# Kernel tuning notes

Measured on AMD Instinct MI355X. Metric: run time of the kernel, lower is better.

Reference implementation:

```python
import jax, jax.numpy as jnp
import numpy as np

EPS = 1e-5

def _ln(x):
    # LayerNorm over last dim, no affine (elementwise_affine=False)
    mu = jnp.mean(x, axis=-1, keepdims=True)
    var = jnp.mean(jnp.square(x - mu), axis=-1, keepdims=True)
    return (x - mu) * jax.lax.rsqrt(var + EPS)

def setup_inputs() -> dict:
    key = jax.random.key(0)
    ks = jax.random.split(key, 6)
    B, L, D = 2, 2048, 2048
    s = 1.0 / np.sqrt(D)
    return {
        "x": jax.random.normal(ks[0], (B, L, D), jnp.float32),
        "Wq": jax.random.normal(ks[1], (D, D), jnp.float32) * s,
        "Wk": jax.random.normal(ks[2], (D, D), jnp.float32) * s,
        "Wv": jax.random.normal(ks[3], (D, D), jnp.float32) * s,
        "Wo": jax.random.normal(ks[4], (D, D), jnp.float32) * s,
        "bo": jnp.zeros((D,), jnp.float32),
    }

def reference(x, Wq, Wk, Wv, Wo, bo):
    B, L, D = x.shape
    H = 16
    hd = D // H
    q = (x @ Wq.T).reshape(B, L, H, hd)
    k = (x @ Wk.T).reshape(B, L, H, hd)
    v = (x @ Wv.T).reshape(B, L, H, hd)
    q = _ln(q)
    k = _ln(k)
    scores = jnp.einsum('blhd,bshd->bhls', q, k) / np.sqrt(hd)
    causal = jnp.tril(jnp.ones((L, L), bool))  # [L, L]
    scores = jnp.where(causal[None, None], scores, -jnp.inf)
    probs = jax.nn.softmax(scores, axis=-1)
    out = jnp.einsum('bhls,bshd->blhd', probs, v).reshape(B, L, D)
    return out @ Wo.T + bo
```

## Files before the change

kernel.cpp:

```cpp
#include <hip/hip_runtime.h>
#include <stdint.h>

typedef unsigned short u16;
typedef __attribute__((ext_vector_type(8))) unsigned short u16x8;
typedef __attribute__((ext_vector_type(8))) __bf16 bf16x8;
typedef __attribute__((ext_vector_type(4))) float f32x4;
typedef __attribute__((ext_vector_type(8))) float f32x8;

#define AS_G __attribute__((address_space(1)))
#define AS_L __attribute__((address_space(3)))

static __device__ __forceinline__ void gload_lds16(const u16* g, u16* l) {
  __builtin_amdgcn_global_load_lds((AS_G void*)(u16*)g, (AS_L void*)l, 16, 0, 0);
}

static __device__ __forceinline__ u16 f2bf(float f) {
  union { float f; unsigned u; } v; v.f = f;
  return (u16)((v.u + 0x7FFFu + ((v.u >> 16) & 1u)) >> 16);
}
static __device__ __forceinline__ float bf2f(u16 b) {
  union { unsigned u; float f; } v; v.u = ((unsigned)b) << 16;
  return v.f;
}
static __device__ __forceinline__ u16 f2bf_trunc(float f) {
  union { float f; unsigned u; } v; v.f = f;
  return (u16)(v.u >> 16);
}

#define BAR() do { asm volatile("" ::: "memory"); __builtin_amdgcn_s_barrier(); asm volatile("" ::: "memory"); } while (0)

__global__ __launch_bounds__(256) void cast_all(
    const float* __restrict__ x, const float* __restrict__ Wq,
    const float* __restrict__ Wk, const float* __restrict__ Wv,
    const float* __restrict__ Wo,
    u16* __restrict__ xb, u16* __restrict__ Wcat, u16* __restrict__ Wob)
{
  const int NX = (4096 * 2048) / 8;
  const int NW = (2048 * 2048) / 8;
  const int total = NX + 4 * NW;
  for (int i = blockIdx.x * 256 + threadIdx.x; i < total; i += gridDim.x * 256) {
    const float* src; u16* dst; int idx;
    if (i < NX)               { src = x;  dst = xb;                 idx = i; }
    else if (i < NX + NW)     { src = Wq; dst = Wcat;               idx = i - NX; }
    else if (i < NX + 2*NW)   { src = Wk; dst = Wcat + 2048*2048;   idx = i - NX - NW; }
    else if (i < NX + 3*NW)   { src = Wv; dst = Wcat + 2*2048*2048; idx = i - NX - 2*NW; }
    else                      { src = Wo; dst = Wob;                idx = i - NX - 3*NW; }
    f32x8 v = *(const f32x8*)(src + (size_t)idx * 8);
    u16x8 o;
    #pragma unroll
    for (int e = 0; e < 8; e++) o[e] = f2bf(v[e]);
    *(u16x8*)(dst + (size_t)idx * 8) = o;
  }
}

__global__ __launch_bounds__(512, 1) void gemm_qkv(
    const u16* __restrict__ A, const u16* __restrict__ B,
    u16* __restrict__ QK, u16* __restrict__ Vt, int K)
{
  __shared__ char SM[98304];
  u16* Asb = (u16*)SM;
  u16* Bsb = (u16*)(SM + 32768);
  const int tid = threadIdx.x, lane = tid & 63, wid = tid >> 6;
  const int wm = wid >> 2, wn = wid & 3;
  const int row0 = blockIdx.x * 128, col0 = blockIdx.y * 256;
  const int NT = K >> 6;

  const int sr  = tid >> 3;
  const int scb = ((tid & 7) * 16) ^ ((sr & 7) << 4);

  auto stA = [&](int buf, int t, int u) {
    const u16* src = A + (size_t)(row0 + u * 64 + sr) * K + t * 64 + (scb >> 1);
    gload_lds16(src, Asb + buf * 8192 + u * 4096 + wid * 512);
  };
  auto stB = [&](int buf, int t, int u) {
    const u16* src = B + (size_t)(col0 + u * 64 + sr) * K + t * 64 + (scb >> 1);
    gload_lds16(src, Bsb + buf * 16384 + u * 4096 + wid * 512);
  };
  auto ldA = [&](int buf, int mf, int k) {
    int ra = wm * 64 + mf * 16 + (lane & 15);
    int bc = (k * 64 + ((lane >> 4) << 4)) ^ ((ra & 7) << 4);
    return *(const bf16x8*)((const char*)Asb + buf * 16384 + ra * 128 + bc);
  };
  auto ldB = [&](int buf, int nf, int k) {
    int rb = wn * 64 + nf * 16 + (lane & 15);
    int bc = (k * 64 + ((lane >> 4) << 4)) ^ ((rb & 7) << 4);
    return *(const bf16x8*)((const char*)Bsb + buf * 32768 + rb * 128 + bc);
  };

  f32x4 acc[4][4] = {};
  bf16x8 breg[4][2];

#define MFMA_PH(mf, x0, x1) \
  do { __builtin_amdgcn_s_setprio(1); \
    _Pragma("unroll") \
    for (int nf = 0; nf < 4; ++nf) { \
      acc[mf][nf] = __builtin_amdgcn_mfma_f32_16x16x32_bf16(x0, breg[nf][0], acc[mf][nf], 0, 0, 0); \
      acc[mf][nf] = __builtin_amdgcn_mfma_f32_16x16x32_bf16(x1, breg[nf][1], acc[mf][nf], 0, 0, 0); \
    } \
    __builtin_amdgcn_s_setprio(0); } while (0)

  stA(0, 0, 0); stA(0, 0, 1);
  stB(0, 0, 0); stB(0, 0, 1); stB(0, 0, 2); stB(0, 0, 3);
  stB(1, 1, 0); stB(1, 1, 1); stB(1, 1, 2); stB(1, 1, 3);
  asm volatile("s_waitcnt vmcnt(4)" ::: "memory");
  BAR();

  for (int it = 0; it < NT / 2; ++it) {
    const int t1  = 2 * it + 1;
    const int pf0 = (2 * it + 2 < NT) ? (2 * it + 2) : (NT - 1);
    const int pf1 = (2 * it + 3 < NT) ? (2 * it + 3) : (NT - 1);
    #pragma unroll
    for (int hf = 0; hf < 2; ++hf) {
      const int cb = hf;
      #pragma unroll
      for (int nf = 0; nf < 4; ++nf) { breg[nf][0] = ldB(cb, nf, 0); breg[nf][1] = ldB(cb, nf, 1); }
      bf16x8 a0 = ldA(cb, 0, 0), a1 = ldA(cb, 0, 1);
      BAR();
      if (hf == 0) { stA(1, t1, 0); stA(1, t1, 1); } else { stA(0, pf0, 0); stA(0, pf0, 1); }
      MFMA_PH(0, a0, a1);
      a0 = ldA(cb, 1, 0); a1 = ldA(cb, 1, 1);
      BAR();
      if (hf == 0) { stB(0, pf0, 0); stB(0, pf0, 1); } else { stB(1, pf1, 0); stB(1, pf1, 1); }
      MFMA_PH(1, a0, a1);
      a0 = ldA(cb, 2, 0); a1 = ldA(cb, 2, 1);
      BAR();
      if (hf == 0) { stB(0, pf0, 2); stB(0, pf0, 3); } else { stB(1, pf1, 2); stB(1, pf1, 3); }
      MFMA_PH(2, a0, a1);
      a0 = ldA(cb, 3, 0); a1 = ldA(cb, 3, 1);
      MFMA_PH(3, a0, a1);
      asm volatile("s_waitcnt vmcnt(4)" ::: "memory");
      BAR();
    }
  }
  asm volatile("s_waitcnt vmcnt(0)" ::: "memory");
  BAR();

  if (col0 < 4096) {
    float* red = (float*)SM;
    #pragma unroll
    for (int mf = 0; mf < 4; ++mf) {
      #pragma unroll
      for (int e = 0; e < 4; ++e) {
        float s = acc[mf][0][e] + acc[mf][1][e] + acc[mf][2][e] + acc[mf][3][e];
        float q = acc[mf][0][e]*acc[mf][0][e] + acc[mf][1][e]*acc[mf][1][e]
                + acc[mf][2][e]*acc[mf][2][e] + acc[mf][3][e]*acc[mf][3][e];
        #pragma unroll
        for (int m = 1; m < 16; m <<= 1) { s += __shfl_xor(s, m); q += __shfl_xor(q, m); }
        if ((lane & 15) == 0) {
          int rl = mf * 16 + (lane >> 4) * 4 + e;
          red[wid * 128 + rl * 2]     = s;
          red[wid * 128 + rl * 2 + 1] = q;
        }
      }
    }
    BAR();
    const float mul = (col0 < 2048) ? (0.08838834764831845f * 1.4426950408889634f) : 1.0f;
    #pragma unroll
    for (int mf = 0; mf < 4; ++mf) {
      #pragma unroll
      for (int e = 0; e < 4; ++e) {
        int rl = mf * 16 + (lane >> 4) * 4 + e;
        float s = red[wid * 128 + rl * 2]     + red[(wid ^ 1) * 128 + rl * 2];
        float q = red[wid * 128 + rl * 2 + 1] + red[(wid ^ 1) * 128 + rl * 2 + 1];
        float mu = s * (1.f / 128.f);
        float var = q * (1.f / 128.f) - mu * mu;
        float rstd = rsqrtf(var + 1e-5f) * mul;
        int r = row0 + wm * 64 + rl;
        #pragma unroll
        for (int nf = 0; nf < 4; ++nf) {
          int c = col0 + wn * 64 + nf * 16 + (lane & 15);
          QK[(size_t)r * 4096 + c] = f2bf((acc[mf][nf][e] - mu) * rstd);
        }
      }
    }
  } else {
    u16* T = (u16*)SM;
    #pragma unroll
    for (int mf = 0; mf < 4; ++mf) {
      #pragma unroll
      for (int nf = 0; nf < 4; ++nf) {
        #pragma unroll
        for (int e = 0; e < 4; ++e) {
          int r = wm * 64 + mf * 16 + (lane >> 4) * 4 + e;
          int c = wn * 64 + nf * 16 + (lane & 15);
          T[c * 136 + r] = f2bf(acc[mf][nf][e]);
        }
      }
    }
    BAR();
    const int dr = tid >> 1, half = tid & 1;
    const int dg = col0 - 4096 + dr;
    const int h = dg >> 7, dd = dg & 127;
    const int b = row0 >> 11;
    const int lb = (row0 & 2047) + half * 64;
    u16* dst = Vt + ((size_t)((b * 16 + h) * 128 + dd)) * 2048 + lb;
    const u16* srcT = T + dr * 136 + half * 64;
    #pragma unroll
    for (int j = 0; j < 8; ++j)
      *(u16x8*)(dst + j * 8) = *(const u16x8*)(srcT + j * 8);
  }
#undef MFMA_PH
}

__global__ __launch_bounds__(512, 2) void gemm_ao(
    const u16* __restrict__ A, const u16* __restrict__ B,
    float* __restrict__ C, const float* __restrict__ bias,
    int M, int N, int K)
{
  __shared__ u16 As[2][256 * 64];
  __shared__ u16 Bs[2][128 * 64];
  const int tid = threadIdx.x, lane = tid & 63, wid = tid >> 6;
  const int wm = wid >> 1, wn = wid & 1;
  const int row0 = blockIdx.y * 256, col0 = blockIdx.x * 128;
  const int NT = K >> 6;

  const int sr  = tid >> 3;
  const int scb = ((tid & 7) * 16) ^ ((sr & 7) << 4);

  auto stA = [&](int buf, int t, int u) {
    const u16* src = A + (size_t)(row0 + u * 64 + sr) * K + t * 64 + (scb >> 1);
    gload_lds16(src, As[buf] + u * 4096 + wid * 512);
  };
  auto stB = [&](int buf, int t, int u) {
    const u16* src = B + (size_t)(col0 + u * 64 + sr) * K + t * 64 + (scb >> 1);
    gload_lds16(src, Bs[buf] + u * 4096 + wid * 512);
  };
  auto ldA = [&](int buf, int mf, int k) {
    int ra = wm * 64 + mf * 16 + (lane & 15);
    int bc = (k * 64 + ((lane >> 4) << 4)) ^ ((ra & 7) << 4);
    return *(const bf16x8*)((const char*)As[buf] + ra * 128 + bc);
  };
  auto ldB = [&](int buf, int nf, int k) {
    int rb = wn * 64 + nf * 16 + (lane & 15);
    int bc = (k * 64 + ((lane >> 4) << 4)) ^ ((rb & 7) << 4);
    return *(const bf16x8*)((const char*)Bs[buf] + rb * 128 + bc);
  };

  f32x4 acc[4][4] = {};
  bf16x8 breg[4][2];

  stA(0, 0, 0); stA(0, 0, 1); stA(0, 0, 2); stA(0, 0, 3);
  stB(0, 0, 0); stB(0, 0, 1);
  stB(1, 1, 0); stB(1, 1, 1);
  asm volatile("s_waitcnt vmcnt(2)" ::: "memory");
  BAR();

  for (int it = 0; it < NT / 2; ++it) {
    const int t1  = 2 * it + 1;
    const int pf0 = (2 * it + 2 < NT) ? (2 * it + 2) : (NT - 1);
    const int pf1 = (2 * it + 3 < NT) ? (2 * it + 3) : (NT - 1);
    #pragma unroll
    for (int hf = 0; hf < 2; ++hf) {
      const int cb = hf;
      #pragma unroll
      for (int nf = 0; nf < 4; ++nf) { breg[nf][0] = ldB(cb, nf, 0); breg[nf][1] = ldB(cb, nf, 1); }
      bf16x8 a0 = ldA(cb, 0, 0), a1 = ldA(cb, 0, 1);
      BAR();
      if (hf == 0) { stA(1, t1, 0); stA(1, t1, 1); } else { stA(0, pf0, 0); stA(0, pf0, 1); }
      __builtin_amdgcn_s_setprio(1);
      #pragma unroll
      for (int nf = 0; nf < 4; ++nf) {
        acc[0][nf] = __builtin_amdgcn_mfma_f32_16x16x32_bf16(a0, breg[nf][0], acc[0][nf], 0, 0, 0);
        acc[0][nf] = __builtin_amdgcn_mfma_f32_16x16x32_bf16(a1, breg[nf][1], acc[0][nf], 0, 0, 0);
      }
      __builtin_amdgcn_s_setprio(0);
      bf16x8 b0 = ldA(cb, 1, 0), b1 = ldA(cb, 1, 1);
      bf16x8 c0 = ldA(cb, 2, 0), c1 = ldA(cb, 2, 1);
      BAR();
      if (hf == 0) { stA(1, t1, 2); stA(1, t1, 3); } else { stA(0, pf0, 2); stA(0, pf0, 3); }
      __builtin_amdgcn_s_setprio(1);
      #pragma unroll
      for (int nf = 0; nf < 4; ++nf) {
        acc[1][nf] = __builtin_amdgcn_mfma_f32_16x16x32_bf16(b0, breg[nf][0], acc[1][nf], 0, 0, 0);
        acc[1][nf] = __builtin_amdgcn_mfma_f32_16x16x32_bf16(b1, breg[nf][1], acc[1][nf], 0, 0, 0);
        acc[2][nf] = __builtin_amdgcn_mfma_f32_16x16x32_bf16(c0, breg[nf][0], acc[2][nf], 0, 0, 0);
        acc[2][nf] = __builtin_amdgcn_mfma_f32_16x16x32_bf16(c1, breg[nf][1], acc[2][nf], 0, 0, 0);
      }
      __builtin_amdgcn_s_setprio(0);
      a0 = ldA(cb, 3, 0); a1 = ldA(cb, 3, 1);
      BAR();
      if (hf == 0) { stB(0, pf0, 0); stB(0, pf0, 1); } else { stB(1, pf1, 0); stB(1, pf1, 1); }
      __builtin_amdgcn_s_setprio(1);
      #pragma unroll
      for (int nf = 0; nf < 4; ++nf) {
        acc[3][nf] = __builtin_amdgcn_mfma_f32_16x16x32_bf16(a0, breg[nf][0], acc[3][nf], 0, 0, 0);
        acc[3][nf] = __builtin_amdgcn_mfma_f32_16x16x32_bf16(a1, breg[nf][1], acc[3][nf], 0, 0, 0);
      }
      __builtin_amdgcn_s_setprio(0);
      asm volatile("s_waitcnt vmcnt(2)" ::: "memory");
      BAR();
    }
  }
  asm volatile("s_waitcnt vmcnt(0)" ::: "memory");

  #pragma unroll
  for (int mf = 0; mf < 4; ++mf) {
    #pragma unroll
    for (int nf = 0; nf < 4; ++nf) {
      #pragma unroll
      for (int e = 0; e < 4; ++e) {
        int r = row0 + wm * 64 + mf * 16 + (lane >> 4) * 4 + e;
        int c = col0 + wn * 64 + nf * 16 + (lane & 15);
        C[(size_t)r * N + c] = acc[mf][nf][e] + bias[c];
      }
    }
  }
}

static __device__ __forceinline__ void stage_k_tile(
    const u16* __restrict__ QK, int b, int h, int j0, u16* Kbuf, int tid, int wid)
{
  #pragma unroll
  for (int i = 0; i < 4; i++) {
    int c = i * 256 + tid;
    int r = c >> 4, ob = (c & 15) * 16;
    int cb = ob ^ ((r & 7) << 4);
    const u16* g = QK + (size_t)(b*2048 + j0 + r) * 4096 + 2048 + h*128 + (cb >> 1);
    gload_lds16(g, Kbuf + (i * 256 + wid * 64) * 8);
  }
}
static __device__ __forceinline__ void stage_v_tile(
    const u16* __restrict__ Vt, int b, int h, int j0, u16* Vbuf, int tid, int wid)
{
  #pragma unroll
  for (int i = 0; i < 4; i++) {
    int c = i * 256 + tid;
    int r = c >> 3, ob = (c & 7) * 16;
    int cb = ob ^ ((r & 7) << 4);
    const u16* g = Vt + (size_t)((b*16 + h) * 128 + r) * 2048 + j0 + (cb >> 1);
    gload_lds16(g, Vbuf + (i * 256 + wid * 64) * 8);
  }
}

__global__ __launch_bounds__(256, 2) void attn(
    const u16* __restrict__ QK, const u16* __restrict__ Vt, u16* __restrict__ AO)
{
  const int flat = blockIdx.x;
  const int xcd = flat & 7;
  const int j   = flat >> 3;
  const int k   = j >> 1, odd = j & 1;
  int qt, inst;
  if (k < 16) { qt = odd ? 15 - k : k;      inst = odd ? 1 : 0; }
  else        { qt = odd ? k - 16 : 31 - k; inst = odd ? 3 : 2; }
  const int hb = xcd * 4 + inst;
  const int h = hb & 15, b = hb >> 4;
  const int tid = threadIdx.x, lane = tid & 63, wid = tid >> 6;

  __shared__ u16 Ks[2][64 * 128];
  __shared__ u16 Vs[2][128 * 64];
  __shared__ u16 Ps[4][32 * 64];

  const int l0 = qt * 128;
  const int ntile = 2 * qt + 2;

  bf16x8 qa[2][4];
  #pragma unroll
  for (int mt = 0; mt < 2; mt++) {
    const u16* qrow = QK + (size_t)(b*2048 + l0 + wid*32 + mt*16 + (lane & 15)) * 4096
                      + h*128 + (lane >> 4) * 8;
    #pragma unroll
    for (int ks = 0; ks < 4; ks++) qa[mt][ks] = *(const bf16x8*)(qrow + ks * 32);
  }

  f32x4 o[2][8] = {};
  float lrun[8];
  #pragma unroll
  for (int i = 0; i < 8; i++) lrun[i] = 0.f;

  stage_v_tile(Vt, b, h, 0, Vs[0], tid, wid);
  stage_k_tile(QK, b, h, 0, Ks[0], tid, wid);
  int cur = 0;

  for (int t = 0; t < ntile; t++) {
    const int j0 = t * 64;
    if (t + 1 < ntile) {
      stage_v_tile(Vt, b, h, (t + 1) * 64, Vs[cur ^ 1], tid, wid);
      stage_k_tile(QK, b, h, (t + 1) * 64, Ks[cur ^ 1], tid, wid);
      asm volatile("s_waitcnt vmcnt(8)" ::: "memory");
    } else {
      asm volatile("s_waitcnt vmcnt(0)" ::: "memory");
    }
    __builtin_amdgcn_s_barrier();
    asm volatile("" ::: "memory");

    const bool skip = (t == ntile - 1) && (wid < 2);
    if (!skip) {
      f32x4 s[2][4] = {};
      const char* Kc = (const char*)Ks[cur];
      __builtin_amdgcn_s_setprio(1);
      #pragma unroll
      for (int nt = 0; nt < 4; nt++) {
        #pragma unroll
        for (int ks = 0; ks < 4; ks++) {
          int r = nt * 16 + (lane & 15);
          int cb = ks * 64 + (lane >> 4) * 16;
          bf16x8 kb = *(const bf16x8*)(Kc + r * 256 + (cb ^ ((lane & 7) << 4)));
          s[0][nt] = __builtin_amdgcn_mfma_f32_16x16x32_bf16(qa[0][ks], kb, s[0][nt], 0, 0, 0);
          s[1][nt] = __builtin_amdgcn_mfma_f32_16x16x32_bf16(qa[1][ks], kb, s[1][nt], 0, 0, 0);
        }
      }
      __builtin_amdgcn_s_setprio(0);

      if (t >= ntile - 2) {
        #pragma unroll
        for (int mt = 0; mt < 2; mt++) {
          #pragma unroll
          for (int nt = 0; nt < 4; nt++) {
            #pragma unroll
            for (int e = 0; e < 4; e++) {
              int ig = l0 + wid * 32 + mt * 16 + (lane >> 4) * 4 + e;
              int jg = j0 + nt * 16 + (lane & 15);
              if (jg > ig) s[mt][nt][e] = -1e30f;
            }
          }
        }
      }

      char* PsW = (char*)Ps[wid];
      #pragma unroll
      for (int mt = 0; mt < 2; mt++) {
        #pragma unroll
        for (int nt = 0; nt < 4; nt++) {
          #pragma unroll
          for (int e = 0; e < 4; e++) {
            float p = exp2f(s[mt][nt][e]);
            lrun[mt * 4 + e] += p;
            int i_ = mt * 16 + (lane >> 4) * 4 + e;
            int jb = (nt * 16 + (lane & 15)) * 2;
            *(u16*)(PsW + i_ * 128 + (jb ^ ((i_ & 7) << 4))) = f2bf_trunc(p);
          }
        }
      }

      const char* Vc = (const char*)Vs[cur];
      __builtin_amdgcn_s_setprio(1);
      #pragma unroll
      for (int ks = 0; ks < 2; ks++) {
        int jb = ks * 64 + (lane >> 4) * 16;
        bf16x8 pa[2];
        #pragma unroll
        for (int mt = 0; mt < 2; mt++) {
          int ir = mt * 16 + (lane & 15);
          pa[mt] = *(const bf16x8*)(PsW + ir * 128 + (jb ^ ((ir & 7) << 4)));
        }
        #pragma unroll
        for (int dt = 0; dt < 8; dt++) {
          int dr = dt * 16 + (lane & 15);
          bf16x8 vb = *(const bf16x8*)(Vc + dr * 128 + (jb ^ ((lane & 7) << 4)));
          o[0][dt] = __builtin_amdgcn_mfma_f32_16x16x32_bf16(pa[0], vb, o[0][dt], 0, 0, 0);
          o[1][dt] = __builtin_amdgcn_mfma_f32_16x16x32_bf16(pa[1], vb, o[1][dt], 0, 0, 0);
        }
      }
      __builtin_amdgcn_s_setprio(0);
    }

    asm volatile("s_waitcnt lgkmcnt(0)" ::: "memory");
    __builtin_amdgcn_s_barrier();
    asm volatile("" ::: "memory");
    cur ^= 1;
  }

  #pragma unroll
  for (int mt = 0; mt < 2; mt++) {
    #pragma unroll
    for (int e = 0; e < 4; e++) {
      float l = lrun[mt * 4 + e];
      l += __shfl_xor(l, 1);
      l += __shfl_xor(l, 2);
      l += __shfl_xor(l, 4);
      l += __shfl_xor(l, 8);
      float inv = 1.0f / l;
      int rglob = b * 2048 + l0 + wid * 32 + mt * 16 + (lane >> 4) * 4 + e;
      #pragma unroll
      for (int dt = 0; dt < 8; dt++)
        AO[(size_t)rglob * 2048 + h * 128 + dt * 16 + (lane & 15)] = f2bf(o[mt][dt][e] * inv);
    }
  }
}

extern "C" void kernel_launch(void* const* d_in, const int* in_sizes, int n_in,
                              void* d_out, int out_size, void* d_ws, size_t ws_size,
                              hipStream_t stream)
{
  const float* x  = (const float*)d_in[0];
  const float* Wq = (const float*)d_in[1];
  const float* Wk = (const float*)d_in[2];
  const float* Wv = (const float*)d_in[3];
  const float* Wo = (const float*)d_in[4];
  const float* bo = (const float*)d_in[5];

  char* ws = (char*)d_ws;
  u16* xb   = (u16*)(ws);
  u16* Wcat = (u16*)(ws + 16777216);
  u16* Wob  = (u16*)(ws + 16777216 + 25165824);
  u16* QK   = (u16*)(ws + 16777216 + 25165824 + 8388608);
  u16* Vt   = (u16*)(ws + 16777216 + 25165824 + 8388608 + 33554432);
  u16* AO   = xb;

  cast_all<<<dim3(2048), dim3(256), 0, stream>>>(x, Wq, Wk, Wv, Wo, xb, Wcat, Wob);
  gemm_qkv<<<dim3(32, 24), dim3(512), 0, stream>>>(xb, Wcat, QK, Vt, 2048);
  attn<<<dim3(512), dim3(256), 0, stream>>>(QK, Vt, AO);
  gemm_ao<<<dim3(16, 16), dim3(512), 0, stream>>>(AO, Wob, (float*)d_out, bo, 4096, 2048, 2048);
}
```

Measured before the change: 248.1 us.

## Enlarge QKV GEMM tile to 256x256 with restructured pipelined phases

The QKV projection GEMM block tile grows from 128x256 to 256x256, so each wave computes 128x64 and the grid halves to 16x24 blocks. The main loop is rewritten into phases that each handle two M-fragments, with an explicit lgkmcnt wait and a sched_barrier before the MFMAs. The V-transpose epilogue now runs in two passes through LDS so the transposed tile fits. The aim is more data reuse per byte loaded. In exchange it roughly doubles accumulator registers, raises LDS use to 128KB, and launch_bounds(512,2) is likely unattainable, which may cause spills. The smaller grid also risks poor CU fill.

```diff
diff --git a/kernel.cpp b/kernel.cpp
--- a/kernel.cpp
+++ b/kernel.cpp
@@ -53,16 +53,16 @@
   }
 }
 
-__global__ __launch_bounds__(512, 1) void gemm_qkv(
+__global__ __launch_bounds__(512, 2) void gemm_qkv(
     const u16* __restrict__ A, const u16* __restrict__ B,
     u16* __restrict__ QK, u16* __restrict__ Vt, int K)
 {
-  __shared__ char SM[98304];
+  __shared__ char SM[131072];
   u16* Asb = (u16*)SM;
-  u16* Bsb = (u16*)(SM + 32768);
+  u16* Bsb = (u16*)(SM + 65536);
   const int tid = threadIdx.x, lane = tid & 63, wid = tid >> 6;
   const int wm = wid >> 2, wn = wid & 3;
-  const int row0 = blockIdx.x * 128, col0 = blockIdx.y * 256;
+  const int row0 = blockIdx.x * 256, col0 = blockIdx.y * 256;
   const int NT = K >> 6;
 
   const int sr  = tid >> 3;
@@ -70,16 +70,16 @@
 
   auto stA = [&](int buf, int t, int u) {
     const u16* src = A + (size_t)(row0 + u * 64 + sr) * K + t * 64 + (scb >> 1);
-    gload_lds16(src, Asb + buf * 8192 + u * 4096 + wid * 512);
+    gload_lds16(src, Asb + buf * 16384 + u * 4096 + wid * 512);
   };
   auto stB = [&](int buf, int t, int u) {
     const u16* src = B + (size_t)(col0 + u * 64 + sr) * K + t * 64 + (scb >> 1);
     gload_lds16(src, Bsb + buf * 16384 + u * 4096 + wid * 512);
   };
   auto ldA = [&](int buf, int mf, int k) {
-    int ra = wm * 64 + mf * 16 + (lane & 15);
+    int ra = wm * 128 + mf * 16 + (lane & 15);
     int bc = (k * 64 + ((lane >> 4) << 4)) ^ ((ra & 7) << 4);
-    return *(const bf16x8*)((const char*)Asb + buf * 16384 + ra * 128 + bc);
+    return *(const bf16x8*)((const char*)Asb + buf * 32768 + ra * 128 + bc);
   };
   auto ldB = [&](int buf, int nf, int k) {
     int rb = wn * 64 + nf * 16 + (lane & 15);
@@ -87,58 +87,61 @@
     return *(const bf16x8*)((const char*)Bsb + buf * 32768 + rb * 128 + bc);
   };
 
-  f32x4 acc[4][4] = {};
+  f32x4 acc[8][4] = {};
   bf16x8 breg[4][2];
 
-#define MFMA_PH(mf, x0, x1) \
-  do { __builtin_amdgcn_s_setprio(1); \
+#define PH(cb, q, STAGE, DOVM) \
+  { bf16x8 a0 = ldA(cb, 2*(q), 0),   a1 = ldA(cb, 2*(q), 1); \
+    bf16x8 a2 = ldA(cb, 2*(q)+1, 0), a3 = ldA(cb, 2*(q)+1, 1); \
+    STAGE; \
+    BAR(); \
+    asm volatile("s_waitcnt lgkmcnt(0)" ::: "memory"); \
+    __builtin_amdgcn_sched_barrier(0); \
+    __builtin_amdgcn_s_setprio(1); \
     _Pragma("unroll") \
     for (int nf = 0; nf < 4; ++nf) { \
-      acc[mf][nf] = __builtin_amdgcn_mfma_f32_16x16x32_bf16(x0, breg[nf][0], acc[mf][nf], 0, 0, 0); \
-      acc[mf][nf] = __builtin_amdgcn_mfma_f32_16x16x32_bf16(x1, breg[nf][1], acc[mf][nf], 0, 0, 0); \
+      acc[2*(q)][nf]   = __builtin_amdgcn_mfma_f32_16x16x32_bf16(a0, breg[nf][0], acc[2*(q)][nf], 0, 0, 0); \
+      acc[2*(q)][nf]   = __builtin_amdgcn_mfma_f32_16x16x32_bf16(a1, breg[nf][1], acc[2*(q)][nf], 0, 0, 0); \
+      acc[2*(q)+1][nf] = __builtin_amdgcn_mfma_f32_16x16x32_bf16(a2, breg[nf][0], acc[2*(q)+1][nf], 0, 0, 0); \
+      acc[2*(q)+1][nf] = __builtin_amdgcn_mfma_f32_16x16x32_bf16(a3, breg[nf][1], acc[2*(q)+1][nf], 0, 0, 0); \
     } \
-    __builtin_amdgcn_s_setprio(0); } while (0)
-
-  stA(0, 0, 0); stA(0, 0, 1);
+    __builtin_amdgcn_s_setprio(0); \
+    DOVM; \
+    BAR(); }
+#define VM4 asm volatile("s_waitcnt vmcnt(4)" ::: "memory")
+
+  stA(0, 0, 0); stA(0, 0, 1); stA(0, 0, 2); stA(0, 0, 3);
   stB(0, 0, 0); stB(0, 0, 1); stB(0, 0, 2); stB(0, 0, 3);
   stB(1, 1, 0); stB(1, 1, 1); stB(1, 1, 2); stB(1, 1, 3);
   asm volatile("s_waitcnt vmcnt(4)" ::: "memory");
   BAR();
 
-  for (int it = 0; it < NT / 2; ++it) {
-    const int t1  = 2 * it + 1;
-    const int pf0 = (2 * it + 2 < NT) ? (2 * it + 2) : (NT - 1);
-    const int pf1 = (2 * it + 3 < NT) ? (2 * it + 3) : (NT - 1);
-    #pragma unroll
-    for (int hf = 0; hf < 2; ++hf) {
-      const int cb = hf;
-      #pragma unroll
-      for (int nf = 0; nf < 4; ++nf) { breg[nf][0] = ldB(cb, nf, 0); breg[nf][1] = ldB(cb, nf, 1); }
-      bf16x8 a0 = ldA(cb, 0, 0), a1 = ldA(cb, 0, 1);
-      BAR();
-      if (hf == 0) { stA(1, t1, 0); stA(1, t1, 1); } else { stA(0, pf0, 0); stA(0, pf0, 1); }
-      MFMA_PH(0, a0, a1);
-      a0 = ldA(cb, 1, 0); a1 = ldA(cb, 1, 1);
-      BAR();
-      if (hf == 0) { stB(0, pf0, 0); stB(0, pf0, 1); } else { stB(1, pf1, 0); stB(1, pf1, 1); }
-      MFMA_PH(1, a0, a1);
-      a0 = ldA(cb, 2, 0); a1 = ldA(cb, 2, 1);
-      BAR();
-      if (hf == 0) { stB(0, pf0, 2); stB(0, pf0, 3); } else { stB(1, pf1, 2); stB(1, pf1, 3); }
-      MFMA_PH(2, a0, a1);
-      a0 = ldA(cb, 3, 0); a1 = ldA(cb, 3, 1);
-      MFMA_PH(3, a0, a1);
-      asm volatile("s_waitcnt vmcnt(4)" ::: "memory");
-      BAR();
-    }
-  }
+  for (int i = 0; i < NT / 2; ++i) {
+    const int t1 = 2 * i + 1;
+    const int t2 = (2 * i + 2 < NT) ? 2 * i + 2 : NT - 1;
+    const int t3 = (2 * i + 3 < NT) ? 2 * i + 3 : NT - 1;
+    #pragma unroll
+    for (int nf = 0; nf < 4; ++nf) { breg[nf][0] = ldB(0, nf, 0); breg[nf][1] = ldB(0, nf, 1); }
+    PH(0, 0, { stA(1, t1, 0); stA(1, t1, 1); }, );
+    PH(0, 1, { stA(1, t1, 2); stA(1, t1, 3); }, );
+    PH(0, 2, { stB(0, t2, 0); stB(0, t2, 1); }, );
+    PH(0, 3, { stB(0, t2, 2); stB(0, t2, 3); }, VM4);
+    #pragma unroll
+    for (int nf = 0; nf < 4; ++nf) { breg[nf][0] = ldB(1, nf, 0); breg[nf][1] = ldB(1, nf, 1); }
+    PH(1, 0, { stA(0, t2, 0); stA(0, t2, 1); }, );
+    PH(1, 1, { stA(0, t2, 2); stA(0, t2, 3); }, );
+    PH(1, 2, { stB(1, t3, 0); stB(1, t3, 1); }, );
+    PH(1, 3, { stB(1, t3, 2); stB(1, t3, 3); }, VM4);
+  }
+#undef PH
+#undef VM4
   asm volatile("s_waitcnt vmcnt(0)" ::: "memory");
   BAR();
 
   if (col0 < 4096) {
     float* red = (float*)SM;
     #pragma unroll
-    for (int mf = 0; mf < 4; ++mf) {
+    for (int mf = 0; mf < 8; ++mf) {
       #pragma unroll
       for (int e = 0; e < 4; ++e) {
         float s = acc[mf][0][e] + acc[mf][1][e] + acc[mf][2][e] + acc[mf][3][e];
@@ -148,24 +151,24 @@
         for (int m = 1; m < 16; m <<= 1) { s += __shfl_xor(s, m); q += __shfl_xor(q, m); }
         if ((lane & 15) == 0) {
           int rl = mf * 16 + (lane >> 4) * 4 + e;
-          red[wid * 128 + rl * 2]     = s;
-          red[wid * 128 + rl * 2 + 1] = q;
+          red[wid * 256 + rl * 2]     = s;
+          red[wid * 256 + rl * 2 + 1] = q;
         }
       }
     }
     BAR();
     const float mul = (col0 < 2048) ? (0.08838834764831845f * 1.4426950408889634f) : 1.0f;
     #pragma unroll
-    for (int mf = 0; mf < 4; ++mf) {
+    for (int mf = 0; mf < 8; ++mf) {
       #pragma unroll
       for (int e = 0; e < 4; ++e) {
         int rl = mf * 16 + (lane >> 4) * 4 + e;
-        float s = red[wid * 128 + rl * 2]     + red[(wid ^ 1) * 128 + rl * 2];
-        float q = red[wid * 128 + rl * 2 + 1] + red[(wid ^ 1) * 128 + rl * 2 + 1];
+        float s = red[wid * 256 + rl * 2]     + red[(wid ^ 1) * 256 + rl * 2];
+        float q = red[wid * 256 + rl * 2 + 1] + red[(wid ^ 1) * 256 + rl * 2 + 1];
         float mu = s * (1.f / 128.f);
         float var = q * (1.f / 128.f) - mu * mu;
         float rstd = rsqrtf(var + 1e-5f) * mul;
-        int r = row0 + wm * 64 + rl;
+        int r = row0 + wm * 128 + rl;
         #pragma unroll
         for (int nf = 0; nf < 4; ++nf) {
           int c = col0 + wn * 64 + nf * 16 + (lane & 15);
@@ -175,31 +178,35 @@
     }
   } else {
     u16* T = (u16*)SM;
-    #pragma unroll
-    for (int mf = 0; mf < 4; ++mf) {
-      #pragma unroll
-      for (int nf = 0; nf < 4; ++nf) {
-        #pragma unroll
-        for (int e = 0; e < 4; ++e) {
-          int r = wm * 64 + mf * 16 + (lane >> 4) * 4 + e;
-          int c = wn * 64 + nf * 16 + (lane & 15);
-          T[c * 136 + r] = f2bf(acc[mf][nf][e]);
-        }
-      }
-    }
-    BAR();
-    const int dr = tid >> 1, half = tid & 1;
-    const int dg = col0 - 4096 + dr;
-    const int h = dg >> 7, dd = dg & 127;
     const int b = row0 >> 11;
-    const int lb = (row0 & 2047) + half * 64;
-    u16* dst = Vt + ((size_t)((b * 16 + h) * 128 + dd)) * 2048 + lb;
-    const u16* srcT = T + dr * 136 + half * 64;
-    #pragma unroll
-    for (int j = 0; j < 8; ++j)
-      *(u16x8*)(dst + j * 8) = *(const u16x8*)(srcT + j * 8);
-  }
-#undef MFMA_PH
+    #pragma unroll
+    for (int pass = 0; pass < 2; ++pass) {
+      if ((wn >> 1) == pass) {
+        #pragma unroll
+        for (int mf = 0; mf < 8; ++mf)
+          #pragma unroll
+          for (int nf = 0; nf < 4; ++nf)
+            #pragma unroll
+            for (int e = 0; e < 4; ++e) {
+              int r = wm * 128 + mf * 16 + (lane >> 4) * 4 + e;
+              int c = (wn & 1) * 64 + nf * 16 + (lane & 15);
+              T[c * 264 + r] = f2bf(acc[mf][nf][e]);
+            }
+      }
+      BAR();
+      {
+        const int c = tid & 127, seg = tid >> 7;
+        const int dg = col0 - 4096 + pass * 128 + c;
+        const int h = dg >> 7, dd = dg & 127;
+        u16* dst = Vt + ((size_t)((b * 16 + h) * 128 + dd)) * 2048 + (row0 & 2047) + seg * 64;
+        const u16* srcT = T + c * 264 + seg * 64;
+        #pragma unroll
+        for (int jj = 0; jj < 8; ++jj)
+          *(u16x8*)(dst + jj * 8) = *(const u16x8*)(srcT + jj * 8);
+      }
+      BAR();
+    }
+  }
 }
 
 __global__ __launch_bounds__(512, 2) void gemm_ao(
@@ -498,7 +505,7 @@
   u16* AO   = xb;
 
   cast_all<<<dim3(2048), dim3(256), 0, stream>>>(x, Wq, Wk, Wv, Wo, xb, Wcat, Wob);
-  gemm_qkv<<<dim3(32, 24), dim3(512), 0, stream>>>(xb, Wcat, QK, Vt, 2048);
+  gemm_qkv<<<dim3(16, 24), dim3(512), 0, stream>>>(xb, Wcat, QK, Vt, 2048);
   attn<<<dim3(512), dim3(256), 0, stream>>>(QK, Vt, AO);
   gemm_ao<<<dim3(16, 16), dim3(512), 0, stream>>>(AO, Wob, (float*)d_out, bo, 4096, 2048, 2048);
 }
```

Result: slower. 255.9 us (+3.1%).
